# Kernel tuning notes

Hardware: AMD Instinct MI355X
Metric: run time of the kernel (lower is better)

## Reference

```python
import math
import jax, jax.numpy as jnp
import numpy as np
from jax import lax

B, IMG, CIN, ED, TD, M = 32, 224, 3, 64, 64, 32
DILATIONS = (1, 2, 3, 4)
KS, STRIDE = 7, 4


def _conv2d(x, w, b, stride, pad, dil=1):
    y = lax.conv_general_dilated(x, w, (stride, stride), [(pad, pad), (pad, pad)],
                                 rhs_dilation=(dil, dil),
                                 dimension_numbers=('NCHW', 'OIHW', 'NCHW'))
    return y + b[None, :, None, None]


def _ln(x, g, b):
    mu = x.mean(-1, keepdims=True)
    var = ((x - mu) ** 2).mean(-1, keepdims=True)
    return (x - mu) / jnp.sqrt(var + 1e-5) * g + b


def setup_inputs() -> dict:
    key = jax.random.key(0)
    ks = jax.random.split(key, 25)
    s = 0.05
    rn = lambda k, shp: (jax.random.normal(k, shp) * s).astype(jnp.float32)
    inp = {}
    inp['x'] = jax.random.normal(ks[0], (B, CIN, IMG, IMG), dtype=jnp.float32)
    # PRM dilated conv weights (stacked over 4 dilations)
    inp['prm_w'] = rn(ks[1], (4, ED, CIN, KS, KS))
    inp['prm_b'] = rn(ks[2], (4, ED))
    # PCM stem: conv-SiLU, conv-BN-SiLU, conv-SiLU
    inp['pcm_w1'] = rn(ks[3], (ED, CIN, 3, 3))
    inp['pcm_b1'] = rn(ks[4], (ED,))
    inp['pcm_w2'] = rn(ks[5], (ED, ED, 3, 3))
    inp['pcm_b2'] = rn(ks[6], (ED,))
    inp['bn_g'] = 1.0 + rn(ks[7], (ED,))
    inp['bn_b'] = rn(ks[8], (ED,))
    inp['bn_mean'] = rn(ks[9], (ED,))
    inp['bn_var'] = jax.random.uniform(ks[10], (ED,), minval=0.5, maxval=1.5).astype(jnp.float32)
    inp['pcm_w3'] = rn(ks[11], (TD, ED, 3, 3))
    inp['pcm_b3'] = rn(ks[12], (TD,))
    # Token_performer params (dim = 4*ED = 256, emb = TD = 64, m = 32)
    dim = 4 * ED
    inp['ln1_g'] = 1.0 + rn(ks[13], (dim,))
    inp['ln1_b'] = rn(ks[14], (dim,))
    inp['kqv_w'] = rn(ks[15], (3 * TD, dim))
    inp['kqv_b'] = rn(ks[16], (3 * TD,))
    # orthogonal random-feature matrix, rows orthonormal, scaled by sqrt(m)
    a = np.random.default_rng(0).normal(size=(TD, TD))
    qmat, _ = np.linalg.qr(a)
    inp['w_perf'] = jnp.asarray(qmat[:M] * math.sqrt(M), dtype=jnp.float32)
    inp['proj_w'] = rn(ks[17], (TD, TD))
    inp['proj_b'] = rn(ks[18], (TD,))
    inp['ln2_g'] = 1.0 + rn(ks[19], (TD,))
    inp['ln2_b'] = rn(ks[20], (TD,))
    inp['mlp_w1'] = rn(ks[21], (TD, TD))
    inp['mlp_b1'] = rn(ks[22], (TD,))
    inp['mlp_w2'] = rn(ks[23], (TD, TD))
    inp['mlp_b2'] = rn(ks[24], (TD,))
    inp['H'] = IMG
    inp['W'] = IMG
    return inp


def reference(x, prm_w, prm_b, pcm_w1, pcm_b1, pcm_w2, pcm_b2, bn_g, bn_b, bn_mean,
              bn_var, pcm_w3, pcm_b3, ln1_g, ln1_b, kqv_w, kqv_b, w_perf, proj_w,
              proj_b, ln2_g, ln2_b, mlp_w1, mlp_b1, mlp_w2, mlp_b2, H, W):
    Bx = x.shape[0]
    Hp, Wp = H // STRIDE, W // STRIDE
    # --- PRM: parallel dilated Conv2d + GELU branches ---
    branches = []
    for i, d in enumerate(DILATIONS):  # fixed small set of structurally distinct convs
        pad = math.ceil(((KS - 1) * d + 1 - STRIDE) / 2)
        branches.append(jax.nn.gelu(_conv2d(x, prm_w[i], prm_b[i], STRIDE, pad, d),
                                    approximate=False))
    y = jnp.stack(branches, axis=1)  # [B, 4, ED, Hp, Wp]
    prm_x = y.reshape(Bx, len(DILATIONS) * ED, Hp * Wp).transpose(0, 2, 1)  # [B, N, 256]
    # --- PCM stem: conv-SiLU / conv-BN-SiLU / conv-SiLU (eval-mode BN) ---
    c = jax.nn.silu(_conv2d(x, pcm_w1, pcm_b1, 2, 1))
    c = _conv2d(c, pcm_w2, pcm_b2, 2, 1)
    inv = (bn_g / jnp.sqrt(bn_var + 1e-5))[None, :, None, None]
    c = (c - bn_mean[None, :, None, None]) * inv + bn_b[None, :, None, None]
    c = jax.nn.silu(c)
    c = jax.nn.silu(_conv2d(c, pcm_w3, pcm_b3, 1, 1))  # [B, TD, Hp, Wp]
    convX = c.transpose(0, 2, 3, 1).reshape(Bx, Hp * Wp, TD)
    # --- Performer kernelized attention ---
    xn = _ln(prm_x, ln1_g, ln1_b)
    kqv = xn @ kqv_w.T + kqv_b
    k, q, v = kqv[..., :TD], kqv[..., TD:2 * TD], kqv[..., 2 * TD:]

    def prm_exp(z):
        xd = 0.5 * (z * z).sum(-1, keepdims=True)          # [B, N, 1]
        wtx = jnp.einsum('bti,mi->btm', z, w_perf)          # [B, N, M]
        return jnp.exp(wtx - xd) / math.sqrt(M)

    kp, qp = prm_exp(k), prm_exp(q)                         # [B, N, M]
    D = jnp.einsum('btm,bm->bt', qp, kp.sum(axis=1))[..., None]  # [B, N, 1]
    kptv = jnp.einsum('btn,btm->bnm', v, kp)                # [B, TD, M]
    ya = jnp.einsum('btm,bnm->btn', qp, kptv) / (D + 1e-8)  # [B, N, TD]
    ya = v + ya @ proj_w.T + proj_b
    # --- combine + MLP block ---
    xo = ya + convX
    h = _ln(xo, ln2_g, ln2_b)
    h = jax.nn.gelu(h @ mlp_w1.T + mlp_b1, approximate=False) @ mlp_w2.T + mlp_b2
    return xo + h
```

## Files before the change

### kernel.cpp

```cpp
#include <hip/hip_runtime.h>
#include <hip/hip_bf16.h>
#include <cstddef>

#define BB    32
#define IMG   224
#define CIN   3
#define ED    64
#define TD    64
#define MM    32
#define HP    56
#define TT    3136
#define C4    256
#define KQVN  192

typedef __attribute__((ext_vector_type(8))) short bf16x8;
typedef __attribute__((ext_vector_type(4))) float f32x4;

#define OFF_CONVX  0u
#define OFF_XN     6422528u
#define OFF_C2B    6422528u
#define OFF_C1B    19267584u
#define OFF_V      19267584u
#define OFF_KP     25690112u
#define OFF_QP     28901376u
#define OFF_PART   32112640u
#define OFF_KPTV   33161216u
#define OFF_KPSP   (OFF_KPTV + 32768u)
#define OFF_WPJB   (OFF_KPTV + 49152u)
#define OFF_WM1B   (OFF_KPTV + 51200u)
#define OFF_WM2B   (OFF_KPTV + 53248u)
#define OFF_WPFH   (OFF_KPTV + 55296u)
#define OFF_WPFL   (OFF_KPTV + 56320u)
#define OFF_KPSUM  33226752u
#define OFF_WPT    (OFF_PART)
#define OFF_WKB    (OFF_PART + 37632u)
#define OFF_WC2B   (OFF_PART + 62208u)
#define OFF_WT3B   (OFF_PART + 80640u)
#define OFF_WC1B   (OFF_PART + 99072u)

__device__ __forceinline__ float geluf(float v){
  return 0.5f*v*(1.f + erff(v*0.70710678118654752f));
}
__device__ __forceinline__ float siluf(float v){
// ... 42 lines not shown
  } else if (idx < 162560){
    int i5 = idx - 160512;
    int oc = i5 >> 5, k = i5 & 31;
    float v = 0.f;
    if (k < 27) v = pcm_w1[oc*27 + k];
    wc1b[i5] = __float2bfloat16(v);
  } else if (idx < 166656){
    wpjb[idx - 162560] = __float2bfloat16(proj_w[idx - 162560]);
  } else if (idx < 170752){
    wm1b[idx - 166656] = __float2bfloat16(mlp_w1[idx - 166656]);
  } else if (idx < 174848){
    wm2b[idx - 170752] = __float2bfloat16(mlp_w2[idx - 170752]);
  } else if (idx < 176896){
    int i6 = idx - 174848;
    wpfh[i6] = __float2bfloat16(wperf[i6]);
  } else if (idx < 178944){
    int i7 = idx - 176896;
    float v = wperf[i7];
    float h = bf2f(bfbits(v));
    wpfl[i7] = __float2bfloat16(v - h);
  }
}

__global__ __launch_bounds__(256) void k_conv1(
    const float* __restrict__ x, const __hip_bfloat16* __restrict__ wc1b,
    const float* __restrict__ bias, __hip_bfloat16* __restrict__ c1b)
{
  __shared__ __align__(16) ushort xs[3*17*18];
  __shared__ __align__(16) ushort As[64*40];
  const int t = threadIdx.x;
  const int b = blockIdx.y;
  const int th = blockIdx.x/14, tw = blockIdx.x - th*14;
  const int oh0 = th*8, ow0 = tw*8;
  const int ih0 = oh0*2 - 1, iw0 = ow0*2 - 1;
  const int w = t>>6, lane = t&63, l15 = lane&15, hi = lane>>4;

  const float* xb = x + (size_t)b*CIN*IMG*IMG;
  for (int idx = t; idx < 918; idx += 256){
    int ci = idx/306, rem = idx - ci*306;
    int r = rem/18, c = rem - r*18;
    float v = 0.f;
    int ih = ih0 + r, iw = iw0 + c;
    if (c < 17 && (unsigned)ih < 224u && (unsigned)iw < 224u)
      v = xb[(ci*IMG+ih)*IMG+iw];
    xs[idx] = bfbits(v);
  }
  __syncthreads();
  for (int idx = t; idx < 2048; idx += 256){
    int pos = idx >> 5, k = idx & 31;
    ushort v = 0;
    if (k < 27){
      int ci = k/9, rem = k - ci*9;
      int kh = rem/3, kw = rem - kh*3;
      v = xs[(ci*17 + (pos>>3)*2 + kh)*18 + (pos&7)*2 + kw];
    }
    As[pos*40 + k] = v;
  }
  __syncthreads();

  float bs4[4];
  #pragma unroll
  for (int nb=0;nb<4;++nb) bs4[nb] = bias[nb*16+l15];
  f32x4 acc[4];
  #pragma unroll
  for (int nb=0;nb<4;++nb) acc[nb] = (f32x4){0.f,0.f,0.f,0.f};
  const ushort* wq = (const ushort*)wc1b;
  {
    bf16x8 a = *(const bf16x8*)&As[(w*16+l15)*40 + hi*8];
    #pragma unroll
    for (int nb=0;nb<4;++nb){
      bf16x8 bv = *(const bf16x8*)&wq[(nb*16+l15)*32 + hi*8];
      acc[nb] = __builtin_amdgcn_mfma_f32_16x16x32_bf16(a, bv, acc[nb], 0, 0, 0);
    }
  }
  #pragma unroll
  for (int nb=0;nb<4;++nb){
    #pragma unroll
    for (int r=0;r<4;++r){
      int row = w*16 + hi*4 + r;
      int oh = oh0 + (row>>3), ow = ow0 + (row&7);
      c1b[(((size_t)b*112+oh)*112+ow)*64 + nb*16+l15] =
        __float2bfloat16(siluf(acc[nb][r] + bs4[nb]));
    }
  }
}

__global__ __launch_bounds__(256) void k_conv2(
    const __hip_bfloat16* __restrict__ c1b, const __hip_bfloat16* __restrict__ wc2b,
    const float* __restrict__ bias, const float* __restrict__ g,
    const float* __restrict__ bb, const float* __restrict__ mean,
    const float* __restrict__ var, __hip_bfloat16* __restrict__ c2b)
{
  __shared__ __align__(16) ushort xs[17*17*72];
  const int b = blockIdx.y;
  const int th = blockIdx.x/7, tw = blockIdx.x - th*7;
  const int oh0 = th*8, ow0 = tw*8;
  const int t = threadIdx.x;
  const int w = t>>6, lane = t&63, l15 = lane&15, hi = lane>>4;

  const int ih0 = oh0*2-1, iw0 = ow0*2-1;
  const ushort* c1u = (const ushort*)c1b;
  for (int seg = t; seg < 2312; seg += 256){
    int pos = seg >> 3, s8 = seg & 7;
    int r = pos/17, c = pos - r*17;
    int ih = ih0 + r, iw = iw0 + c;
    uint4 val = {0,0,0,0};
    if ((unsigned)ih < 112u && (unsigned)iw < 112u)
      val = *(const uint4*)&c1u[(((size_t)b*112+ih)*112+iw)*64 + s8*8];
    *(uint4*)&xs[(r*17+c)*72 + s8*8] = val;
  }
  __syncthreads();

  float bs4[4], iv4[4], mn4[4], bo4[4];
  #pragma unroll
  for (int nb=0;nb<4;++nb){
    int oc = nb*16+l15;
    bs4[nb] = bias[oc];
    iv4[nb] = g[oc]*rsqrtf(var[oc]+1e-5f);
    mn4[nb] = mean[oc];
    bo4[nb] = bb[oc];
  }

  f32x4 acc[4];
  #pragma unroll
  for (int nb=0;nb<4;++nb) acc[nb] = (f32x4){0.f,0.f,0.f,0.f};

  const int p = w*16 + l15, pr = p>>3, pc = p&7;
  const ushort* wq = (const ushort*)wc2b;

  for (int ks=0; ks<18; ++ks){
    const int k0 = ks*32 + hi*8;
    const int khkw = k0 >> 6, ci0 = k0 & 63;
    const int kh = khkw/3, kw = khkw - kh*3;
    bf16x8 a = *(const bf16x8*)&xs[((2*pr+kh)*17 + 2*pc+kw)*72 + ci0];
    #pragma unroll
    for (int nb=0;nb<4;++nb){
      bf16x8 bv = *(const bf16x8*)&wq[(nb*16+l15)*576 + k0];
      acc[nb] = __builtin_amdgcn_mfma_f32_16x16x32_bf16(a, bv, acc[nb], 0, 0, 0);
    }
  }

  #pragma unroll
  for (int nb=0;nb<4;++nb){
    #pragma unroll
    for (int r=0;r<4;++r){
      int pp = w*16 + hi*4 + r;
      int oh = oh0 + (pp>>3), ow = ow0 + (pp&7);
      float vv = acc[nb][r] + bs4[nb];
      vv = (vv - mn4[nb])*iv4[nb] + bo4[nb];
      c2b[(((size_t)b*56+oh)*56+ow)*64 + nb*16+l15] = __float2bfloat16(siluf(vv));
    }
  }
}

__global__ __launch_bounds__(256) void k_conv3(
    const __hip_bfloat16* __restrict__ c2b, const __hip_bfloat16* __restrict__ wt3b,
    const float* __restrict__ bias, __hip_bfloat16* __restrict__ convXb)
{
  __shared__ __align__(16) ushort xs[10*12*72];
  const int b = blockIdx.y;
  const int th = blockIdx.x/7, tw = blockIdx.x - th*7;
  const int oh0 = th*8, ow0 = tw*8;
  const int t = threadIdx.x;
  const int w = t>>6, lane = t&63, l15 = lane&15, hi = lane>>4;

  const ushort* c2u = (const ushort*)c2b;
  for (int seg = t; seg < 960; seg += 256){
    int pos = seg >> 3, s8 = seg & 7;
    int r = pos/12, c = pos - r*12;
    int ih = oh0 - 1 + r, iw = ow0 - 1 + c;
    uint4 val = {0,0,0,0};
    if ((unsigned)ih < 56u && (unsigned)iw < 56u)
      val = *(const uint4*)&c2u[(((size_t)b*56+ih)*56+iw)*64 + s8*8];
    *(uint4*)&xs[(r*12+c)*72 + s8*8] = val;
  }
  __syncthreads();

  float bs4[4];
  #pragma unroll
  for (int nb=0;nb<4;++nb) bs4[nb] = bias[nb*16+l15];

  f32x4 acc[4];
  #pragma unroll
  for (int nb=0;nb<4;++nb) acc[nb] = (f32x4){0.f,0.f,0.f,0.f};

  const int p = w*16 + l15, pr = p>>3, pc = p&7;
  const ushort* wq = (const ushort*)wt3b;

  for (int ks=0; ks<18; ++ks){
    const int k0 = ks*32 + hi*8;
    const int khkw = k0 >> 6, ci0 = k0 & 63;
    const int kh = khkw/3, kw = khkw - kh*3;
    bf16x8 a = *(const bf16x8*)&xs[((pr+kh)*12 + pc+kw)*72 + ci0];
    #pragma unroll
    for (int nb=0;nb<4;++nb){
      bf16x8 bv = *(const bf16x8*)&wq[(nb*16+l15)*576 + k0];
      acc[nb] = __builtin_amdgcn_mfma_f32_16x16x32_bf16(a, bv, acc[nb], 0, 0, 0);
    }
  }

  #pragma unroll
  for (int nb=0;nb<4;++nb){
    #pragma unroll
    for (int r=0;r<4;++r){
      int pp = w*16 + hi*4 + r;
      int oh = oh0 + (pp>>3), ow = ow0 + (pp&7);
      int s = oh*HP + ow;
      convXb[((size_t)b*TT + s)*64 + nb*16+l15] =
        __float2bfloat16(siluf(acc[nb][r] + bs4[nb]));
    }
  }
}

#define LOADX(PH) do{ const float4* xr_ = (const float4*)(rowb + (PH)*20); \
  *(float4*)&X[0]=xr_[0]; *(float4*)&X[4]=xr_[1]; *(float4*)&X[8]=xr_[2]; \
  *(float4*)&X[12]=xr_[3]; *(float4*)&X[16]=xr_[4]; }while(0)
#define TAP(KW,Q0) do{ const float wv_ = wrow[(KW)*64]; \
  v[0]+=wv_*X[(Q0)+0];  v[1]+=wv_*X[(Q0)+1];  v[2]+=wv_*X[(Q0)+2];  v[3]+=wv_*X[(Q0)+3]; \
  v[4]+=wv_*X[(Q0)+4];  v[5]+=wv_*X[(Q0)+5];  v[6]+=wv_*X[(Q0)+6];  v[7]+=wv_*X[(Q0)+7]; \
  v[8]+=wv_*X[(Q0)+8];  v[9]+=wv_*X[(Q0)+9];  v[10]+=wv_*X[(Q0)+10]; v[11]+=wv_*X[(Q0)+11]; \
  v[12]+=wv_*X[(Q0)+12]; v[13]+=wv_*X[(Q0)+13]; }while(0)

template<int D>
__device__ __forceinline__ void prm_core(const float* __restrict__ xt2,
    const float* __restrict__ wq, float v[14])
{
  constexpr int R0 = 12 - 3*D;
  #pragma unroll 1
  for (int ci=0; ci<3; ++ci){
    #pragma unroll 1
    for (int kh=0; kh<7; ++kh){
      const float* rowb = xt2 + ci*2000 + (R0 + kh*D)*80;
      const float* wrow = wq + ((ci*7+kh)*7)*64;
      float X[20];
      if constexpr (D == 1){
        LOADX(0); TAP(3,3);
        LOADX(1); TAP(0,2); TAP(4,3);
        LOADX(2); TAP(1,2); TAP(5,3);
        LOADX(3); TAP(2,2); TAP(6,3);
      } else if constexpr (D == 2){
        LOADX(0); TAP(1,2); TAP(3,3); TAP(5,4);
        LOADX(2); TAP(0,1); TAP(2,2); TAP(4,3); TAP(6,4);
      } else if constexpr (D == 3){
        LOADX(0); TAP(3,3);
        LOADX(1); TAP(2,2); TAP(6,5);
        LOADX(2); TAP(1,1); TAP(5,4);
        LOADX(3); TAP(0,0); TAP(4,3);
      } else {
        LOADX(0); TAP(0,0); TAP(1,1); TAP(2,2); TAP(3,3); TAP(4,4); TAP(5,5); TAP(6,6);
      }
    }
  }
}

__global__ __launch_bounds__(256) void k_prm_ln(
    const float* __restrict__ x, const float* __restrict__ wpt,
    const float* __restrict__ prm_b, const float* __restrict__ ln_g,
    const float* __restrict__ ln_b, __hip_bfloat16* __restrict__ xn, int b0)
{
  __shared__ __align__(16) float xt2[6000];
  __shared__ float wred[4][14][2];
  const int t = threadIdx.x;
  const int b = blockIdx.y + b0;
  const int oh  = blockIdx.x >> 2;
  const int owt = blockIdx.x & 3;
  const int ow0 = owt*14;
  const int ih0 = oh*4 - 11;
  const int iw0 = ow0*4 - 11;

  const float* xb = x + (size_t)b*CIN*IMG*IMG;
  for (int idx = t; idx < 6000; idx += 256){
    int ci  = idx / 2000;
    int rem = idx - ci*2000;
    int r   = rem / 80;
    int cc  = rem - r*80;
    int ih = ih0 + r, iw = iw0 + cc;
    float val = 0.f;
    if ((unsigned)ih < (unsigned)IMG && (unsigned)iw < (unsigned)IMG)
      val = xb[(ci*IMG+ih)*IMG+iw];
    xt2[(ci*25 + r)*80 + (cc&3)*20 + (cc>>2)] = val;
  }
  __syncthreads();

  const int i = t >> 6, lane = t & 63;
  float v[14];
  const float bi = prm_b[i*64+lane];
  #pragma unroll
  for (int p=0;p<14;++p) v[p] = bi;
  const float* wq = wpt + (i*147)*64 + lane;

  if      (i == 0) prm_core<1>(xt2, wq, v);
  else if (i == 1) prm_core<2>(xt2, wq, v);
  else if (i == 2) prm_core<3>(xt2, wq, v);
  else             prm_core<4>(xt2, wq, v);

  #pragma unroll
  for (int p=0;p<14;++p) v[p] = geluf(v[p]);
  #pragma unroll
  for (int p=0;p<14;++p){
    float s1 = v[p], s2 = v[p]*v[p];
    #pragma unroll
    for (int o=32;o;o>>=1){
      s1 += __shfl_xor(s1, o, 64);
      s2 += __shfl_xor(s2, o, 64);
    }
    if (lane == 0){ wred[i][p][0] = s1; wred[i][p][1] = s2; }
  }
  __syncthreads();
  const float lg = ln_g[t], lb = ln_b[t];
  const int s_base = oh*HP + ow0;
  #pragma unroll
  for (int p=0;p<14;++p){
    float S1 = wred[0][p][0]+wred[1][p][0]+wred[2][p][0]+wred[3][p][0];
    float S2 = wred[0][p][1]+wred[1][p][1]+wred[2][p][1]+wred[3][p][1];
    float mu = S1*(1.f/256.f);
    float rs = rsqrtf(S2*(1.f/256.f) - mu*mu + 1e-5f);
    float outv = (v[p]-mu)*rs*lg + lb;
    xn[((size_t)(b*TT + s_base + p))*256 + t] = __float2bfloat16(outv);
  }
}

__global__ __launch_bounds__(256) void k_kqv_perf(
    const __hip_bfloat16* __restrict__ xn, const __hip_bfloat16* __restrict__ wkb,
    const float* __restrict__ kqv_b,
    const __hip_bfloat16* __restrict__ wpfh, const __hip_bfloat16* __restrict__ wpfl,
    float* __restrict__ v_g, float* __restrict__ kp, float* __restrict__ qp)
{
  __shared__ __align__(16) char smem[36864];
  __shared__ __align__(16) ushort wph[32*72];
  __shared__ __align__(16) ushort wpl[32*72];
  __shared__ float kqvb_s[192];
  __shared__ float xd_s[128];
  ushort* As  = (ushort*)smem;
  ushort* Bs  = (ushort*)(smem + 9216);
  ushort* zhb = (ushort*)smem;
  ushort* zlb = (ushort*)(smem + 18432);

  const int t = threadIdx.x;
  const int m0 = blockIdx.x*64;
  const int w = t >> 6, lane = t & 63;
  const int l15 = lane & 15, hi = lane >> 4;

  const ushort* wph_g = (const ushort*)wpfh;
  const ushort* wpl_g = (const ushort*)wpfl;
  for (int idx = t; idx < 2048; idx += 256){
    int row = idx >> 6, c = idx & 63;
    wph[row*72 + c] = wph_g[idx];
    wpl[row*72 + c] = wpl_g[idx];
  }
// ... 29 lines not shown
      for (int nb=0;nb<12;++nb){
        bf16x8 bv = *(const bf16x8*)&Bs[(nb*16 + l15)*72 + ks*32 + hi*8];
        acc[nb] = __builtin_amdgcn_mfma_f32_16x16x32_bf16(a, bv, acc[nb], 0, 0, 0);
      }
    }
    __syncthreads();
  }

  #pragma unroll
  for (int nb=0;nb<12;++nb){
    int col = nb*16 + l15;
    float bias = kqvb_s[col];
    #pragma unroll
    for (int r=0;r<4;++r){
      int row = w*16 + hi*4 + r;
      float val = acc[nb][r] + bias;
      if (col < 128){
        int zrow = (col >> 6)*64 + row;
        int zc = col & 63;
        ushort zh = bfbits(val);
        zhb[zrow*72 + zc] = zh;
        zlb[zrow*72 + zc] = bfbits(val - bf2f(zh));
      } else {
        v_g[((size_t)(m0+row))*64 + (col-128)] = val;
      }
    }
  }
  __syncthreads();

  if (t < 128){
    float s = 0.f;
    #pragma unroll
    for (int c8=0;c8<8;++c8){
      bf16x8 zh8 = *(const bf16x8*)&zhb[t*72 + c8*8];
      bf16x8 zl8 = *(const bf16x8*)&zlb[t*72 + c8*8];
      #pragma unroll
      for (int j=0;j<8;++j){
        float z = bf2f((ushort)zh8[j]) + bf2f((ushort)zl8[j]);
        s += z*z;
      }
    }
    xd_s[t] = 0.5f*s;
  }
  __syncthreads();

  f32x4 accd[2][2];
  #pragma unroll
// ... 8 lines not shown
      bf16x8 ah = *(const bf16x8*)&zhb[(rb*16 + l15)*72 + ks*32 + hi*8];
      bf16x8 al = *(const bf16x8*)&zlb[(rb*16 + l15)*72 + ks*32 + hi*8];
      #pragma unroll
      for (int nb=0;nb<2;++nb){
        bf16x8 bh = *(const bf16x8*)&wph[(nb*16 + l15)*72 + ks*32 + hi*8];
        bf16x8 bl = *(const bf16x8*)&wpl[(nb*16 + l15)*72 + ks*32 + hi*8];
        accd[ri][nb] = __builtin_amdgcn_mfma_f32_16x16x32_bf16(ah, bh, accd[ri][nb], 0, 0, 0);
        accd[ri][nb] = __builtin_amdgcn_mfma_f32_16x16x32_bf16(al, bh, accd[ri][nb], 0, 0, 0);
        accd[ri][nb] = __builtin_amdgcn_mfma_f32_16x16x32_bf16(ah, bl, accd[ri][nb], 0, 0, 0);
      }
    }
  }
  #pragma unroll
  for (int ri=0;ri<2;++ri){
    const int rb = 2*w + ri;
    #pragma unroll
    for (int nb=0;nb<2;++nb){
      const int m = nb*16 + l15;
      #pragma unroll
      for (int r=0;r<4;++r){
        int row = rb*16 + hi*4 + r;
        int wh = row >> 6, pos = row & 63;
        float outv = expf(accd[ri][nb][r] - xd_s[row]) * 0.17677669529663687f;
        float* dst = wh ? qp : kp;
        dst[((size_t)(m0+pos))*32 + m] = outv;
      }
    }
  }
}

__global__ __launch_bounds__(256) void k_kptv(
    const float* __restrict__ v_g, const float* __restrict__ kp,
    float* __restrict__ part, float* __restrict__ kpsum_part)
{
  __shared__ __align__(16) ushort vT[64*232];
  __shared__ __align__(16) ushort kpT[32*232];
  __shared__ float ksh[8][32];
  const int b = blockIdx.y, g = blockIdx.x;
  const int t = threadIdx.x;
  const int w = t>>6, lane = t&63, l15 = lane&15, hi = lane>>4;
  const int t0 = g*196;

  for (int idx = t; idx < 14336; idx += 256){
    int tt = idx >> 6, n = idx & 63;
    float vv = (tt < 196) ? v_g[((size_t)b*TT + t0 + tt)*64 + n] : 0.f;
    vT[n*232 + tt] = bfbits(vv);
  }
  for (int idx = t; idx < 7168; idx += 256){
    int tt = idx >> 5, m = idx & 31;
    float kv = (tt < 196) ? kp[((size_t)b*TT + t0 + tt)*32 + m] : 0.f;
    kpT[m*232 + tt] = bfbits(kv);
  }
  __syncthreads();

  f32x4 accp[2];
  accp[0] = (f32x4){0.f,0.f,0.f,0.f};
  accp[1] = (f32x4){0.f,0.f,0.f,0.f};
  for (int ks=0; ks<7; ++ks){
    bf16x8 a = *(const bf16x8*)&vT[(w*16+l15)*232 + ks*32 + hi*8];
    #pragma unroll
    for (int nt=0; nt<2; ++nt){
      bf16x8 bv = *(const bf16x8*)&kpT[(nt*16+l15)*232 + ks*32 + hi*8];
      accp[nt] = __builtin_amdgcn_mfma_f32_16x16x32_bf16(a, bv, accp[nt], 0, 0, 0);
    }
  }
  #pragma unroll
  for (int nt=0;nt<2;++nt){
    #pragma unroll
    for (int r=0;r<4;++r){
      int row = w*16 + hi*4 + r;
      int col = nt*16 + l15;
      part[(((size_t)g*BB + b)*64 + row)*MM + col] = accp[nt][r];
    }
  }
  {
    int m = t & 31, h8 = t >> 5;
    float s = 0.f;
    int lo = h8*25, hic = lo+25 < 196 ? lo+25 : 196;
    for (int tt = lo; tt < hic; ++tt){
      s += bf2f(kpT[m*232 + tt]);
    }
    ksh[h8][m] = s;
  }
  __syncthreads();
  if (t < 32){
    float s = 0.f;
    #pragma unroll
    for (int j=0;j<8;++j) s += ksh[j][t];
    kpsum_part[(size_t)g*1024 + b*32 + t] = s;
  }
}

__global__ __launch_bounds__(256) void k_kptv_red(
    const float* __restrict__ part, const float* __restrict__ kpsum_part,
    __hip_bfloat16* __restrict__ kptvb, float* __restrict__ kpsum)
{
  const int t = threadIdx.x;
  const int idx = blockIdx.x*256 + t;
  float a = 0.f;
  #pragma unroll
  for (int g=0; g<16; ++g) a += part[(size_t)g*65536 + idx];
  kptvb[idx] = __float2bfloat16(a);
  if (blockIdx.x < 4){
    int kidx = blockIdx.x*256 + t;
    float s = 0.f;
    #pragma unroll
    for (int g=0; g<16; ++g) s += kpsum_part[(size_t)g*1024 + kidx];
    kpsum[kidx] = s;
  }
}

__global__ __launch_bounds__(256) void k_attn_mlp(
    const float* __restrict__ v_g, const float* __restrict__ qp,
    const float* __restrict__ kpsum, const __hip_bfloat16* __restrict__ kptvb,
    const __hip_bfloat16* __restrict__ wpjb, const float* __restrict__ projb,
    const __hip_bfloat16* __restrict__ convXb,
    const float* __restrict__ ln2_g, const float* __restrict__ ln2_b,
    const __hip_bfloat16* __restrict__ wm1b, const float* __restrict__ b1,
    const __hip_bfloat16* __restrict__ wm2b, const float* __restrict__ b2,
    float* __restrict__ out)
{
  __shared__ __align__(16) char smem[64512];
  ushort* qpb = (ushort*)smem;
  ushort* ktb = (ushort*)(smem + 5120);
  ushort* pjw = (ushort*)(smem + 10240);
  ushort* hb  = (ushort*)smem;
  ushort* t2  = (ushort*)(smem + 19456);
  ushort* w1b = (ushort*)(smem + 28672);
  ushort* w2b = (ushort*)(smem + 37888);
  float*  xosh= (float*)(smem + 47104);
  __shared__ float Ds[64];
  __shared__ float Dp[4][64];
  __shared__ float ks_s[32], pjb_s[64], b1_s[64], b2_s[64], g2_s[64], bb2_s[64];

  const int t = threadIdx.x;
  const int b = blockIdx.y;
  const int p0 = blockIdx.x*64;
  const int w = t>>6, lane = t&63, l15 = lane&15, hi = lane>>4;

  const float* qpg = qp + ((size_t)b*TT + p0)*32;
  for (int idx = t; idx < 2048; idx += 256)
    qpb[(idx>>5)*40 + (idx&31)] = bfbits(qpg[idx]);
  const ushort* ktg = (const ushort*)kptvb + (size_t)b*2048;
  for (int idx = t; idx < 2048; idx += 256)
    ktb[(idx>>5)*40 + (idx&31)] = ktg[idx];
  const ushort* pju = (const ushort*)wpjb;
  const ushort* w1u = (const ushort*)wm1b;
  const ushort* w2u = (const ushort*)wm2b;
  for (int idx = t; idx < 4096; idx += 256){
    pjw[(idx>>6)*72 + (idx&63)] = pju[idx];
    w1b[(idx>>6)*72 + (idx&63)] = w1u[idx];
    w2b[(idx>>6)*72 + (idx&63)] = w2u[idx];
  }
  if (t < 32) ks_s[t] = kpsum[b*MM + t];
  if (t < 64){
    pjb_s[t] = projb[t]; b1_s[t] = b1[t]; b2_s[t] = b2[t];
    g2_s[t] = ln2_g[t];  bb2_s[t] = ln2_b[t];
  }
  __syncthreads();

  {
    int pos = t & 63, grp = t >> 6;
    float s = 0.f;
    #pragma unroll
    for (int j=0;j<8;++j){
// ... 20 lines not shown
  #pragma unroll
  for (int nb=0;nb<4;++nb){
    #pragma unroll
    for (int r=0;r<4;++r){
      int row = w*16 + hi*4 + r;
      t2[row*72 + nb*16 + l15] = bfbits(acc1[nb][r] / Ds[row]);
    }
  }
  __syncthreads();

  f32x4 acc2[4];
  #pragma unroll
  for (int nb=0;nb<4;++nb) acc2[nb] = (f32x4){0.f,0.f,0.f,0.f};
  #pragma unroll
  for (int ks=0; ks<2; ++ks){
    bf16x8 a2 = *(const bf16x8*)&t2[(w*16 + l15)*72 + ks*32 + hi*8];
    #pragma unroll
    for (int nb=0;nb<4;++nb){
      bf16x8 bv2 = *(const bf16x8*)&pjw[(nb*16 + l15)*72 + ks*32 + hi*8];
      acc2[nb] = __builtin_amdgcn_mfma_f32_16x16x32_bf16(a2, bv2, acc2[nb], 0, 0, 0);
    }
  }
  const ushort* cxu = (const ushort*)convXb;
  #pragma unroll
  for (int nb=0;nb<4;++nb){
    #pragma unroll
    for (int r=0;r<4;++r){
      int row = w*16 + hi*4 + r;
      int col = nb*16 + l15;
      const size_t off = ((size_t)b*TT + p0 + row)*64 + col;
      xosh[row*68 + col] = v_g[off] + acc2[nb][r] + pjb_s[col] + bf2f(cxu[off]);
    }
  }
  __syncthreads();

  {
    const int n = t & 63, p = t >> 6;
    const float g2 = g2_s[n], bb2 = bb2_s[n];
    for (int sp=0; sp<16; ++sp){
      const int pos = sp*4 + p;
      const float xv = xosh[pos*68 + n];
      float s1 = xv, s2 = xv*xv;
      #pragma unroll
      for (int o=32;o;o>>=1){
        s1 += __shfl_xor(s1, o, 64);
        s2 += __shfl_xor(s2, o, 64);
      }
      float mu = s1*(1.f/64.f);
      float rs = rsqrtf(s2*(1.f/64.f) - mu*mu + 1e-5f);
      t2[pos*72 + n] = bfbits((xv - mu)*rs*g2 + bb2);
    }
  }
  __syncthreads();

// ... 58 lines not shown
  const float* pcm_b2 = (const float*)d_in[6];
  const float* bn_g   = (const float*)d_in[7];
  const float* bn_b   = (const float*)d_in[8];
  const float* bn_mean= (const float*)d_in[9];
  const float* bn_var = (const float*)d_in[10];
  const float* pcm_w3 = (const float*)d_in[11];
  const float* pcm_b3 = (const float*)d_in[12];
  const float* ln1_g  = (const float*)d_in[13];
  const float* ln1_b  = (const float*)d_in[14];
  const float* kqv_w  = (const float*)d_in[15];
  const float* kqv_b  = (const float*)d_in[16];
  const float* w_perf = (const float*)d_in[17];
  const float* proj_w = (const float*)d_in[18];
  const float* proj_b = (const float*)d_in[19];
  const float* ln2_g  = (const float*)d_in[20];
  const float* ln2_b  = (const float*)d_in[21];
  const float* mlp_w1 = (const float*)d_in[22];
  const float* mlp_b1 = (const float*)d_in[23];
  const float* mlp_w2 = (const float*)d_in[24];
  const float* mlp_b2 = (const float*)d_in[25];

  float* ws = (float*)d_ws;
  __hip_bfloat16* convXb = (__hip_bfloat16*)(ws + OFF_CONVX);
  __hip_bfloat16* xn  = (__hip_bfloat16*)(ws + OFF_XN);
  __hip_bfloat16* c2b = (__hip_bfloat16*)(ws + OFF_C2B);
  __hip_bfloat16* c1b = (__hip_bfloat16*)(ws + OFF_C1B);
  float* v_g   = ws + OFF_V;
  float* kp    = ws + OFF_KP;
  float* qp    = ws + OFF_QP;
  float* part  = ws + OFF_PART;
  __hip_bfloat16* kptvb = (__hip_bfloat16*)(ws + OFF_KPTV);
  float* kpsum_part = ws + OFF_KPSP;
  float* kpsum = ws + OFF_KPSUM;
  float* wpt   = ws + OFF_WPT;
  __hip_bfloat16* wkb  = (__hip_bfloat16*)(ws + OFF_WKB);
  __hip_bfloat16* wc2b = (__hip_bfloat16*)(ws + OFF_WC2B);
  __hip_bfloat16* wt3b = (__hip_bfloat16*)(ws + OFF_WT3B);
  __hip_bfloat16* wc1b = (__hip_bfloat16*)(ws + OFF_WC1B);
  __hip_bfloat16* wpjb = (__hip_bfloat16*)(ws + OFF_WPJB);
  __hip_bfloat16* wm1b = (__hip_bfloat16*)(ws + OFF_WM1B);
  __hip_bfloat16* wm2b = (__hip_bfloat16*)(ws + OFF_WM2B);
  __hip_bfloat16* wpfh = (__hip_bfloat16*)(ws + OFF_WPFH);
  __hip_bfloat16* wpfl = (__hip_bfloat16*)(ws + OFF_WPFL);
  float* out   = (float*)d_out;

  k_wtrans<<<dim3(699), 256, 0, stream>>>(prm_w, kqv_w, pcm_w2, pcm_w3, pcm_w1,
                                          proj_w, mlp_w1, mlp_w2, w_perf,
                                          wpt, wkb, wc2b, wt3b, wc1b,
                                          wpjb, wm1b, wm2b, wpfh, wpfl);
  k_conv1<<<dim3(196,BB), 256, 0, stream>>>(x, wc1b, pcm_b1, c1b);
  k_conv2<<<dim3(49,BB), 256, 0, stream>>>(c1b, wc2b, pcm_b2, bn_g, bn_b,
                                           bn_mean, bn_var, c2b);
  k_conv3<<<dim3(49,BB), 256, 0, stream>>>(c2b, wt3b, pcm_b3, convXb);
  k_prm_ln<<<dim3(224,16), 256, 0, stream>>>(x, wpt, prm_b, ln1_g, ln1_b, xn, 0);
  k_prm_ln<<<dim3(224,16), 256, 0, stream>>>(x, wpt, prm_b, ln1_g, ln1_b, xn, 16);
  k_kqv_perf<<<dim3(1568), 256, 0, stream>>>(xn, wkb, kqv_b, wpfh, wpfl, v_g, kp, qp);
  k_kptv<<<dim3(16,BB), 256, 0, stream>>>(v_g, kp, part, kpsum_part);
  k_kptv_red<<<dim3(256), 256, 0, stream>>>(part, kpsum_part, kptvb, kpsum);
  k_attn_mlp<<<dim3(49,BB), 256, 0, stream>>>(v_g, qp, kpsum, kptvb, wpjb, proj_b,
                                              convXb, ln2_g, ln2_b, wm1b, mlp_b1,
                                              wm2b, mlp_b2, out);
}
```

Baseline: 484.9 us.

## Merge PRM and conv1 into one launch; store v, kp, qp as bf16

Result: slower. 497.8 us (+2.7%).

```diff
diff --git a/kernel.cpp b/kernel.cpp
--- a/kernel.cpp
+++ b/kernel.cpp
@@ -17,8 +17,8 @@
 typedef __attribute__((ext_vector_type(4))) float f32x4;
 
 #define OFF_CONVX  0u
+#define OFF_C2B    3211264u
 #define OFF_XN     6422528u
-#define OFF_C2B    6422528u
 #define OFF_C1B    19267584u
 #define OFF_V      19267584u
 #define OFF_KP     25690112u
@@ -107,196 +107,6 @@
   }
 }
 
-__global__ __launch_bounds__(256) void k_conv1(
-    const float* __restrict__ x, const __hip_bfloat16* __restrict__ wc1b,
-    const float* __restrict__ bias, __hip_bfloat16* __restrict__ c1b)
-{
-  __shared__ __align__(16) ushort xs[3*17*18];
-  __shared__ __align__(16) ushort As[64*40];
-  const int t = threadIdx.x;
-  const int b = blockIdx.y;
-  const int th = blockIdx.x/14, tw = blockIdx.x - th*14;
-  const int oh0 = th*8, ow0 = tw*8;
-  const int ih0 = oh0*2 - 1, iw0 = ow0*2 - 1;
-  const int w = t>>6, lane = t&63, l15 = lane&15, hi = lane>>4;
-
-  const float* xb = x + (size_t)b*CIN*IMG*IMG;
-  for (int idx = t; idx < 918; idx += 256){
-    int ci = idx/306, rem = idx - ci*306;
-    int r = rem/18, c = rem - r*18;
-    float v = 0.f;
-    int ih = ih0 + r, iw = iw0 + c;
-    if (c < 17 && (unsigned)ih < 224u && (unsigned)iw < 224u)
-      v = xb[(ci*IMG+ih)*IMG+iw];
-    xs[idx] = bfbits(v);
-  }
-  __syncthreads();
-  for (int idx = t; idx < 2048; idx += 256){
-    int pos = idx >> 5, k = idx & 31;
-    ushort v = 0;
-    if (k < 27){
-      int ci = k/9, rem = k - ci*9;
-      int kh = rem/3, kw = rem - kh*3;
-      v = xs[(ci*17 + (pos>>3)*2 + kh)*18 + (pos&7)*2 + kw];
-    }
-    As[pos*40 + k] = v;
-  }
-  __syncthreads();
-
-  float bs4[4];
-  #pragma unroll
-  for (int nb=0;nb<4;++nb) bs4[nb] = bias[nb*16+l15];
-  f32x4 acc[4];
-  #pragma unroll
-  for (int nb=0;nb<4;++nb) acc[nb] = (f32x4){0.f,0.f,0.f,0.f};
-  const ushort* wq = (const ushort*)wc1b;
-  {
-    bf16x8 a = *(const bf16x8*)&As[(w*16+l15)*40 + hi*8];
-    #pragma unroll
-    for (int nb=0;nb<4;++nb){
-      bf16x8 bv = *(const bf16x8*)&wq[(nb*16+l15)*32 + hi*8];
-      acc[nb] = __builtin_amdgcn_mfma_f32_16x16x32_bf16(a, bv, acc[nb], 0, 0, 0);
-    }
-  }
-  #pragma unroll
-  for (int nb=0;nb<4;++nb){
-    #pragma unroll
-    for (int r=0;r<4;++r){
-      int row = w*16 + hi*4 + r;
-      int oh = oh0 + (row>>3), ow = ow0 + (row&7);
-      c1b[(((size_t)b*112+oh)*112+ow)*64 + nb*16+l15] =
-        __float2bfloat16(siluf(acc[nb][r] + bs4[nb]));
-    }
-  }
-}
-
-__global__ __launch_bounds__(256) void k_conv2(
-    const __hip_bfloat16* __restrict__ c1b, const __hip_bfloat16* __restrict__ wc2b,
-    const float* __restrict__ bias, const float* __restrict__ g,
-    const float* __restrict__ bb, const float* __restrict__ mean,
-    const float* __restrict__ var, __hip_bfloat16* __restrict__ c2b)
-{
-  __shared__ __align__(16) ushort xs[17*17*72];
-  const int b = blockIdx.y;
-  const int th = blockIdx.x/7, tw = blockIdx.x - th*7;
-  const int oh0 = th*8, ow0 = tw*8;
-  const int t = threadIdx.x;
-  const int w = t>>6, lane = t&63, l15 = lane&15, hi = lane>>4;
-
-  const int ih0 = oh0*2-1, iw0 = ow0*2-1;
-  const ushort* c1u = (const ushort*)c1b;
-  for (int seg = t; seg < 2312; seg += 256){
-    int pos = seg >> 3, s8 = seg & 7;
-    int r = pos/17, c = pos - r*17;
-    int ih = ih0 + r, iw = iw0 + c;
-    uint4 val = {0,0,0,0};
-    if ((unsigned)ih < 112u && (unsigned)iw < 112u)
-      val = *(const uint4*)&c1u[(((size_t)b*112+ih)*112+iw)*64 + s8*8];
-    *(uint4*)&xs[(r*17+c)*72 + s8*8] = val;
-  }
-  __syncthreads();
-
-  float bs4[4], iv4[4], mn4[4], bo4[4];
-  #pragma unroll
-  for (int nb=0;nb<4;++nb){
-    int oc = nb*16+l15;
-    bs4[nb] = bias[oc];
-    iv4[nb] = g[oc]*rsqrtf(var[oc]+1e-5f);
-    mn4[nb] = mean[oc];
-    bo4[nb] = bb[oc];
-  }
-
-  f32x4 acc[4];
-  #pragma unroll
-  for (int nb=0;nb<4;++nb) acc[nb] = (f32x4){0.f,0.f,0.f,0.f};
-
-  const int p = w*16 + l15, pr = p>>3, pc = p&7;
-  const ushort* wq = (const ushort*)wc2b;
-
-  for (int ks=0; ks<18; ++ks){
-    const int k0 = ks*32 + hi*8;
-    const int khkw = k0 >> 6, ci0 = k0 & 63;
-    const int kh = khkw/3, kw = khkw - kh*3;
-    bf16x8 a = *(const bf16x8*)&xs[((2*pr+kh)*17 + 2*pc+kw)*72 + ci0];
-    #pragma unroll
-    for (int nb=0;nb<4;++nb){
-      bf16x8 bv = *(const bf16x8*)&wq[(nb*16+l15)*576 + k0];
-      acc[nb] = __builtin_amdgcn_mfma_f32_16x16x32_bf16(a, bv, acc[nb], 0, 0, 0);
-    }
-  }
-
-  #pragma unroll
-  for (int nb=0;nb<4;++nb){
-    #pragma unroll
-    for (int r=0;r<4;++r){
-      int pp = w*16 + hi*4 + r;
-      int oh = oh0 + (pp>>3), ow = ow0 + (pp&7);
-      float vv = acc[nb][r] + bs4[nb];
-      vv = (vv - mn4[nb])*iv4[nb] + bo4[nb];
-      c2b[(((size_t)b*56+oh)*56+ow)*64 + nb*16+l15] = __float2bfloat16(siluf(vv));
-    }
-  }
-}
-
-__global__ __launch_bounds__(256) void k_conv3(
-    const __hip_bfloat16* __restrict__ c2b, const __hip_bfloat16* __restrict__ wt3b,
-    const float* __restrict__ bias, __hip_bfloat16* __restrict__ convXb)
-{
-  __shared__ __align__(16) ushort xs[10*12*72];
-  const int b = blockIdx.y;
-  const int th = blockIdx.x/7, tw = blockIdx.x - th*7;
-  const int oh0 = th*8, ow0 = tw*8;
-  const int t = threadIdx.x;
-  const int w = t>>6, lane = t&63, l15 = lane&15, hi = lane>>4;
-
-  const ushort* c2u = (const ushort*)c2b;
-  for (int seg = t; seg < 960; seg += 256){
-    int pos = seg >> 3, s8 = seg & 7;
-    int r = pos/12, c = pos - r*12;
-    int ih = oh0 - 1 + r, iw = ow0 - 1 + c;
-    uint4 val = {0,0,0,0};
-    if ((unsigned)ih < 56u && (unsigned)iw < 56u)
-      val = *(const uint4*)&c2u[(((size_t)b*56+ih)*56+iw)*64 + s8*8];
-    *(uint4*)&xs[(r*12+c)*72 + s8*8] = val;
-  }
-  __syncthreads();
-
-  float bs4[4];
-  #pragma unroll
-  for (int nb=0;nb<4;++nb) bs4[nb] = bias[nb*16+l15];
-
-  f32x4 acc[4];
-  #pragma unroll
-  for (int nb=0;nb<4;++nb) acc[nb] = (f32x4){0.f,0.f,0.f,0.f};
-
-  const int p = w*16 + l15, pr = p>>3, pc = p&7;
-  const ushort* wq = (const ushort*)wt3b;
-
-  for (int ks=0; ks<18; ++ks){
-    const int k0 = ks*32 + hi*8;
-    const int khkw = k0 >> 6, ci0 = k0 & 63;
-    const int kh = khkw/3, kw = khkw - kh*3;
-    bf16x8 a = *(const bf16x8*)&xs[((pr+kh)*12 + pc+kw)*72 + ci0];
-    #pragma unroll
-    for (int nb=0;nb<4;++nb){
-      bf16x8 bv = *(const bf16x8*)&wq[(nb*16+l15)*576 + k0];
-      acc[nb] = __builtin_amdgcn_mfma_f32_16x16x32_bf16(a, bv, acc[nb], 0, 0, 0);
-    }
-  }
-
-  #pragma unroll
-  for (int nb=0;nb<4;++nb){
-    #pragma unroll
-    for (int r=0;r<4;++r){
-      int pp = w*16 + hi*4 + r;
-      int oh = oh0 + (pp>>3), ow = ow0 + (pp&7);
-      int s = oh*HP + ow;
-      convXb[((size_t)b*TT + s)*64 + nb*16+l15] =
-        __float2bfloat16(siluf(acc[nb][r] + bs4[nb]));
-    }
-  }
-}
-
 #define LOADX(PH) do{ const float4* xr_ = (const float4*)(rowb + (PH)*20); \
   *(float4*)&X[0]=xr_[0]; *(float4*)&X[4]=xr_[1]; *(float4*)&X[8]=xr_[2]; \
   *(float4*)&X[12]=xr_[3]; *(float4*)&X[16]=xr_[4]; }while(0)
@@ -338,70 +148,263 @@
   }
 }
 
-__global__ __launch_bounds__(256) void k_prm_ln(
+__global__ __launch_bounds__(256) void k_prm_conv1(
     const float* __restrict__ x, const float* __restrict__ wpt,
     const float* __restrict__ prm_b, const float* __restrict__ ln_g,
-    const float* __restrict__ ln_b, __hip_bfloat16* __restrict__ xn, int b0)
-{
-  __shared__ __align__(16) float xt2[6000];
+    const float* __restrict__ ln_b, __hip_bfloat16* __restrict__ xn,
+    const __hip_bfloat16* __restrict__ wc1b, const float* __restrict__ c1bias,
+    __hip_bfloat16* __restrict__ c1b)
+{
+  __shared__ __align__(16) char fsm[24448];
   __shared__ float wred[4][14][2];
   const int t = threadIdx.x;
-  const int b = blockIdx.y + b0;
-  const int oh  = blockIdx.x >> 2;
-  const int owt = blockIdx.x & 3;
-  const int ow0 = owt*14;
-  const int ih0 = oh*4 - 11;
-  const int iw0 = ow0*4 - 11;
-
-  const float* xb = x + (size_t)b*CIN*IMG*IMG;
-  for (int idx = t; idx < 6000; idx += 256){
-    int ci  = idx / 2000;
-    int rem = idx - ci*2000;
-    int r   = rem / 80;
-    int cc  = rem - r*80;
-    int ih = ih0 + r, iw = iw0 + cc;
-    float val = 0.f;
-    if ((unsigned)ih < (unsigned)IMG && (unsigned)iw < (unsigned)IMG)
-      val = xb[(ci*IMG+ih)*IMG+iw];
-    xt2[(ci*25 + r)*80 + (cc&3)*20 + (cc>>2)] = val;
-  }
-  __syncthreads();
-
-  const int i = t >> 6, lane = t & 63;
-  float v[14];
-  const float bi = prm_b[i*64+lane];
-  #pragma unroll
-  for (int p=0;p<14;++p) v[p] = bi;
-  const float* wq = wpt + (i*147)*64 + lane;
-
-  if      (i == 0) prm_core<1>(xt2, wq, v);
-  else if (i == 1) prm_core<2>(xt2, wq, v);
-  else if (i == 2) prm_core<3>(xt2, wq, v);
-  else             prm_core<4>(xt2, wq, v);
-
-  #pragma unroll
-  for (int p=0;p<14;++p) v[p] = geluf(v[p]);
-  #pragma unroll
-  for (int p=0;p<14;++p){
-    float s1 = v[p], s2 = v[p]*v[p];
-    #pragma unroll
-    for (int o=32;o;o>>=1){
-      s1 += __shfl_xor(s1, o, 64);
-      s2 += __shfl_xor(s2, o, 64);
-    }
-    if (lane == 0){ wred[i][p][0] = s1; wred[i][p][1] = s2; }
-  }
-  __syncthreads();
-  const float lg = ln_g[t], lb = ln_b[t];
-  const int s_base = oh*HP + ow0;
-  #pragma unroll
-  for (int p=0;p<14;++p){
-    float S1 = wred[0][p][0]+wred[1][p][0]+wred[2][p][0]+wred[3][p][0];
-    float S2 = wred[0][p][1]+wred[1][p][1]+wred[2][p][1]+wred[3][p][1];
-    float mu = S1*(1.f/256.f);
-    float rs = rsqrtf(S2*(1.f/256.f) - mu*mu + 1e-5f);
-    float outv = (v[p]-mu)*rs*lg + lb;
-    xn[((size_t)(b*TT + s_base + p))*256 + t] = __float2bfloat16(outv);
+  const int group = blockIdx.x/15, r15 = blockIdx.x - group*15;
+
+  if (r15 < 8){
+    float* xt2 = (float*)fsm;
+    const int pid = group*8 + r15;
+    const int b = pid/224, rest = pid - b*224;
+    const int oh  = rest >> 2;
+    const int owt = rest & 3;
+    const int ow0 = owt*14;
+    const int ih0 = oh*4 - 11;
+    const int iw0 = ow0*4 - 11;
+
+    const float* xb = x + (size_t)b*CIN*IMG*IMG;
+    for (int idx = t; idx < 6000; idx += 256){
+      int ci  = idx / 2000;
+      int rem = idx - ci*2000;
+      int r   = rem / 80;
+      int cc  = rem - r*80;
+      int ih = ih0 + r, iw = iw0 + cc;
+      float val = 0.f;
+      if ((unsigned)ih < (unsigned)IMG && (unsigned)iw < (unsigned)IMG)
+        val = xb[(ci*IMG+ih)*IMG+iw];
+      xt2[(ci*25 + r)*80 + (cc&3)*20 + (cc>>2)] = val;
+    }
+    __syncthreads();
+
+    const int i = t >> 6, lane = t & 63;
+    float v[14];
+    const float bi = prm_b[i*64+lane];
+    #pragma unroll
+    for (int p=0;p<14;++p) v[p] = bi;
+    const float* wq = wpt + (i*147)*64 + lane;
+
+    if      (i == 0) prm_core<1>(xt2, wq, v);
+    else if (i == 1) prm_core<2>(xt2, wq, v);
+    else if (i == 2) prm_core<3>(xt2, wq, v);
+    else             prm_core<4>(xt2, wq, v);
+
+    #pragma unroll
+    for (int p=0;p<14;++p) v[p] = geluf(v[p]);
+    #pragma unroll
+    for (int p=0;p<14;++p){
+      float s1 = v[p], s2 = v[p]*v[p];
+      #pragma unroll
+      for (int o=32;o;o>>=1){
+        s1 += __shfl_xor(s1, o, 64);
+        s2 += __shfl_xor(s2, o, 64);
+      }
+      if (lane == 0){ wred[i][p][0] = s1; wred[i][p][1] = s2; }
+    }
+    __syncthreads();
+    const float lg = ln_g[t], lb = ln_b[t];
+    const int s_base = oh*HP + ow0;
+    #pragma unroll
+    for (int p=0;p<14;++p){
+      float S1 = wred[0][p][0]+wred[1][p][0]+wred[2][p][0]+wred[3][p][0];
+      float S2 = wred[0][p][1]+wred[1][p][1]+wred[2][p][1]+wred[3][p][1];
+      float mu = S1*(1.f/256.f);
+      float rs = rsqrtf(S2*(1.f/256.f) - mu*mu + 1e-5f);
+      float outv = (v[p]-mu)*rs*lg + lb;
+      xn[((size_t)(b*TT + s_base + p))*256 + t] = __float2bfloat16(outv);
+    }
+  } else {
+    ushort* xs = (ushort*)fsm;
+    ushort* As = (ushort*)(fsm + 4096);
+    const int cid = group*7 + (r15 - 8);
+    const int b = cid/196, s196 = cid - b*196;
+    const int th = s196/14, tw = s196 - th*14;
+    const int oh0 = th*8, ow0 = tw*8;
+    const int ih0 = oh0*2 - 1, iw0 = ow0*2 - 1;
+    const int w = t>>6, lane = t&63, l15 = lane&15, hi = lane>>4;
+
+    const float* xb = x + (size_t)b*CIN*IMG*IMG;
+    for (int idx = t; idx < 918; idx += 256){
+      int ci = idx/306, rem = idx - ci*306;
+      int r = rem/18, c = rem - r*18;
+      float v = 0.f;
+      int ih = ih0 + r, iw = iw0 + c;
+      if (c < 17 && (unsigned)ih < 224u && (unsigned)iw < 224u)
+        v = xb[(ci*IMG+ih)*IMG+iw];
+      xs[idx] = bfbits(v);
+    }
+    __syncthreads();
+    for (int idx = t; idx < 2048; idx += 256){
+      int pos = idx >> 5, k = idx & 31;
+      ushort v = 0;
+      if (k < 27){
+        int ci = k/9, rem = k - ci*9;
+        int kh = rem/3, kw = rem - kh*3;
+        v = xs[(ci*17 + (pos>>3)*2 + kh)*18 + (pos&7)*2 + kw];
+      }
+      As[pos*40 + k] = v;
+    }
+    __syncthreads();
+
+    float bs4[4];
+    #pragma unroll
+    for (int nb=0;nb<4;++nb) bs4[nb] = c1bias[nb*16+l15];
+    f32x4 acc[4];
+    #pragma unroll
+    for (int nb=0;nb<4;++nb) acc[nb] = (f32x4){0.f,0.f,0.f,0.f};
+    const ushort* wq = (const ushort*)wc1b;
+    {
+      bf16x8 a = *(const bf16x8*)&As[(w*16+l15)*40 + hi*8];
+      #pragma unroll
+      for (int nb=0;nb<4;++nb){
+        bf16x8 bv = *(const bf16x8*)&wq[(nb*16+l15)*32 + hi*8];
+        acc[nb] = __builtin_amdgcn_mfma_f32_16x16x32_bf16(a, bv, acc[nb], 0, 0, 0);
+      }
+    }
+    #pragma unroll
+    for (int nb=0;nb<4;++nb){
+      #pragma unroll
+      for (int r=0;r<4;++r){
+        int row = w*16 + hi*4 + r;
+        int oh = oh0 + (row>>3), ow = ow0 + (row&7);
+        c1b[(((size_t)b*112+oh)*112+ow)*64 + nb*16+l15] =
+          __float2bfloat16(siluf(acc[nb][r] + bs4[nb]));
+      }
+    }
+  }
+}
+
+__global__ __launch_bounds__(256) void k_conv2(
+    const __hip_bfloat16* __restrict__ c1b, const __hip_bfloat16* __restrict__ wc2b,
+    const float* __restrict__ bias, const float* __restrict__ g,
+    const float* __restrict__ bb, const float* __restrict__ mean,
+    const float* __restrict__ var, __hip_bfloat16* __restrict__ c2b)
+{
+  __shared__ __align__(16) ushort xs[17*17*72];
+  const int b = blockIdx.y;
+  const int th = blockIdx.x/7, tw = blockIdx.x - th*7;
+  const int oh0 = th*8, ow0 = tw*8;
+  const int t = threadIdx.x;
+  const int w = t>>6, lane = t&63, l15 = lane&15, hi = lane>>4;
+
+  const int ih0 = oh0*2-1, iw0 = ow0*2-1;
+  const ushort* c1u = (const ushort*)c1b;
+  for (int seg = t; seg < 2312; seg += 256){
+    int pos = seg >> 3, s8 = seg & 7;
+    int r = pos/17, c = pos - r*17;
+    int ih = ih0 + r, iw = iw0 + c;
+    uint4 val = {0,0,0,0};
+    if ((unsigned)ih < 112u && (unsigned)iw < 112u)
+      val = *(const uint4*)&c1u[(((size_t)b*112+ih)*112+iw)*64 + s8*8];
+    *(uint4*)&xs[(r*17+c)*72 + s8*8] = val;
+  }
+  __syncthreads();
+
+  float bs4[4], iv4[4], mn4[4], bo4[4];
+  #pragma unroll
+  for (int nb=0;nb<4;++nb){
+    int oc = nb*16+l15;
+    bs4[nb] = bias[oc];
+    iv4[nb] = g[oc]*rsqrtf(var[oc]+1e-5f);
+    mn4[nb] = mean[oc];
+    bo4[nb] = bb[oc];
+  }
+
+  f32x4 acc[4];
+  #pragma unroll
+  for (int nb=0;nb<4;++nb) acc[nb] = (f32x4){0.f,0.f,0.f,0.f};
+
+  const int p = w*16 + l15, pr = p>>3, pc = p&7;
+  const ushort* wq = (const ushort*)wc2b;
+
+  for (int ks=0; ks<18; ++ks){
+    const int k0 = ks*32 + hi*8;
+    const int khkw = k0 >> 6, ci0 = k0 & 63;
+    const int kh = khkw/3, kw = khkw - kh*3;
+    bf16x8 a = *(const bf16x8*)&xs[((2*pr+kh)*17 + 2*pc+kw)*72 + ci0];
+    #pragma unroll
+    for (int nb=0;nb<4;++nb){
+      bf16x8 bv = *(const bf16x8*)&wq[(nb*16+l15)*576 + k0];
+      acc[nb] = __builtin_amdgcn_mfma_f32_16x16x32_bf16(a, bv, acc[nb], 0, 0, 0);
+    }
+  }
+
+  #pragma unroll
+  for (int nb=0;nb<4;++nb){
+    #pragma unroll
+    for (int r=0;r<4;++r){
+      int pp = w*16 + hi*4 + r;
+      int oh = oh0 + (pp>>3), ow = ow0 + (pp&7);
+      float vv = acc[nb][r] + bs4[nb];
+      vv = (vv - mn4[nb])*iv4[nb] + bo4[nb];
+      c2b[(((size_t)b*56+oh)*56+ow)*64 + nb*16+l15] = __float2bfloat16(siluf(vv));
+    }
+  }
+}
+
+__global__ __launch_bounds__(256) void k_conv3(
+    const __hip_bfloat16* __restrict__ c2b, const __hip_bfloat16* __restrict__ wt3b,
+    const float* __restrict__ bias, __hip_bfloat16* __restrict__ convXb)
+{
+  __shared__ __align__(16) ushort xs[10*12*72];
+  const int b = blockIdx.y;
+  const int th = blockIdx.x/7, tw = blockIdx.x - th*7;
+  const int oh0 = th*8, ow0 = tw*8;
+  const int t = threadIdx.x;
+  const int w = t>>6, lane = t&63, l15 = lane&15, hi = lane>>4;
+
+  const ushort* c2u = (const ushort*)c2b;
+  for (int seg = t; seg < 960; seg += 256){
+    int pos = seg >> 3, s8 = seg & 7;
+    int r = pos/12, c = pos - r*12;
+    int ih = oh0 - 1 + r, iw = ow0 - 1 + c;
+    uint4 val = {0,0,0,0};
+    if ((unsigned)ih < 56u && (unsigned)iw < 56u)
+      val = *(const uint4*)&c2u[(((size_t)b*56+ih)*56+iw)*64 + s8*8];
+    *(uint4*)&xs[(r*12+c)*72 + s8*8] = val;
+  }
+  __syncthreads();
+
+  float bs4[4];
+  #pragma unroll
+  for (int nb=0;nb<4;++nb) bs4[nb] = bias[nb*16+l15];
+
+  f32x4 acc[4];
+  #pragma unroll
+  for (int nb=0;nb<4;++nb) acc[nb] = (f32x4){0.f,0.f,0.f,0.f};
+
+  const int p = w*16 + l15, pr = p>>3, pc = p&7;
+  const ushort* wq = (const ushort*)wt3b;
+
+  for (int ks=0; ks<18; ++ks){
+    const int k0 = ks*32 + hi*8;
+    const int khkw = k0 >> 6, ci0 = k0 & 63;
+    const int kh = khkw/3, kw = khkw - kh*3;
+    bf16x8 a = *(const bf16x8*)&xs[((pr+kh)*12 + pc+kw)*72 + ci0];
+    #pragma unroll
+    for (int nb=0;nb<4;++nb){
+      bf16x8 bv = *(const bf16x8*)&wq[(nb*16+l15)*576 + k0];
+      acc[nb] = __builtin_amdgcn_mfma_f32_16x16x32_bf16(a, bv, acc[nb], 0, 0, 0);
+    }
+  }
+
+  #pragma unroll
+  for (int nb=0;nb<4;++nb){
+    #pragma unroll
+    for (int r=0;r<4;++r){
+      int pp = w*16 + hi*4 + r;
+      int oh = oh0 + (pp>>3), ow = ow0 + (pp&7);
+      int s = oh*HP + ow;
+      convXb[((size_t)b*TT + s)*64 + nb*16+l15] =
+        __float2bfloat16(siluf(acc[nb][r] + bs4[nb]));
+    }
   }
 }
 
@@ -409,7 +412,8 @@
     const __hip_bfloat16* __restrict__ xn, const __hip_bfloat16* __restrict__ wkb,
     const float* __restrict__ kqv_b,
     const __hip_bfloat16* __restrict__ wpfh, const __hip_bfloat16* __restrict__ wpfl,
-    float* __restrict__ v_g, float* __restrict__ kp, float* __restrict__ qp)
+    __hip_bfloat16* __restrict__ v_g, __hip_bfloat16* __restrict__ kp,
+    __hip_bfloat16* __restrict__ qp)
 {
   __shared__ __align__(16) char smem[36864];
   __shared__ __align__(16) ushort wph[32*72];
@@ -485,7 +489,7 @@
         zhb[zrow*72 + zc] = zh;
         zlb[zrow*72 + zc] = bfbits(val - bf2f(zh));
       } else {
-        v_g[((size_t)(m0+row))*64 + (col-128)] = val;
+        ((ushort*)v_g)[((size_t)(m0+row))*64 + (col-128)] = bfbits(val);
       }
     }
   }
@@ -540,15 +544,15 @@
         int row = rb*16 + hi*4 + r;
         int wh = row >> 6, pos = row & 63;
         float outv = expf(accd[ri][nb][r] - xd_s[row]) * 0.17677669529663687f;
-        float* dst = wh ? qp : kp;
-        dst[((size_t)(m0+pos))*32 + m] = outv;
+        ushort* dst = (ushort*)(wh ? qp : kp);
+        dst[((size_t)(m0+pos))*32 + m] = bfbits(outv);
       }
     }
   }
 }
 
 __global__ __launch_bounds__(256) void k_kptv(
-    const float* __restrict__ v_g, const float* __restrict__ kp,
+    const __hip_bfloat16* __restrict__ v_g, const __hip_bfloat16* __restrict__ kp,
     float* __restrict__ part, float* __restrict__ kpsum_part)
 {
   __shared__ __align__(16) ushort vT[64*232];
@@ -558,16 +562,16 @@
   const int t = threadIdx.x;
   const int w = t>>6, lane = t&63, l15 = lane&15, hi = lane>>4;
   const int t0 = g*196;
+  const ushort* vu = (const ushort*)v_g;
+  const ushort* ku = (const ushort*)kp;
 
   for (int idx = t; idx < 14336; idx += 256){
     int tt = idx >> 6, n = idx & 63;
-    float vv = (tt < 196) ? v_g[((size_t)b*TT + t0 + tt)*64 + n] : 0.f;
-    vT[n*232 + tt] = bfbits(vv);
+    vT[n*232 + tt] = (tt < 196) ? vu[((size_t)b*TT + t0 + tt)*64 + n] : (ushort)0;
   }
   for (int idx = t; idx < 7168; idx += 256){
     int tt = idx >> 5, m = idx & 31;
-    float kv = (tt < 196) ? kp[((size_t)b*TT + t0 + tt)*32 + m] : 0.f;
-    kpT[m*232 + tt] = bfbits(kv);
+    kpT[m*232 + tt] = (tt < 196) ? ku[((size_t)b*TT + t0 + tt)*32 + m] : (ushort)0;
   }
   __syncthreads();
 
@@ -595,9 +599,7 @@
     int m = t & 31, h8 = t >> 5;
     float s = 0.f;
     int lo = h8*25, hic = lo+25 < 196 ? lo+25 : 196;
-    for (int tt = lo; tt < hic; ++tt){
-      s += bf2f(kpT[m*232 + tt]);
-    }
+    for (int tt = lo; tt < hic; ++tt) s += bf2f(kpT[m*232 + tt]);
     ksh[h8][m] = s;
   }
   __syncthreads();
@@ -629,7 +631,7 @@
 }
 
 __global__ __launch_bounds__(256) void k_attn_mlp(
-    const float* __restrict__ v_g, const float* __restrict__ qp,
+    const __hip_bfloat16* __restrict__ v_g, const __hip_bfloat16* __restrict__ qp,
     const float* __restrict__ kpsum, const __hip_bfloat16* __restrict__ kptvb,
     const __hip_bfloat16* __restrict__ wpjb, const float* __restrict__ projb,
     const __hip_bfloat16* __restrict__ convXb,
@@ -656,9 +658,9 @@
   const int p0 = blockIdx.x*64;
   const int w = t>>6, lane = t&63, l15 = lane&15, hi = lane>>4;
 
-  const float* qpg = qp + ((size_t)b*TT + p0)*32;
+  const ushort* qpu = (const ushort*)qp + ((size_t)b*TT + p0)*32;
   for (int idx = t; idx < 2048; idx += 256)
-    qpb[(idx>>5)*40 + (idx&31)] = bfbits(qpg[idx]);
+    qpb[(idx>>5)*40 + (idx&31)] = qpu[idx];
   const ushort* ktg = (const ushort*)kptvb + (size_t)b*2048;
   for (int idx = t; idx < 2048; idx += 256)
     ktb[(idx>>5)*40 + (idx&31)] = ktg[idx];
@@ -725,6 +727,7 @@
     }
   }
   const ushort* cxu = (const ushort*)convXb;
+  const ushort* vu  = (const ushort*)v_g;
   #pragma unroll
   for (int nb=0;nb<4;++nb){
     #pragma unroll
@@ -732,7 +735,7 @@
       int row = w*16 + hi*4 + r;
       int col = nb*16 + l15;
       const size_t off = ((size_t)b*TT + p0 + row)*64 + col;
-      xosh[row*68 + col] = v_g[off] + acc2[nb][r] + pjb_s[col] + bf2f(cxu[off]);
+      xosh[row*68 + col] = bf2f(vu[off]) + acc2[nb][r] + pjb_s[col] + bf2f(cxu[off]);
     }
   }
   __syncthreads();
@@ -837,12 +840,12 @@
 
   float* ws = (float*)d_ws;
   __hip_bfloat16* convXb = (__hip_bfloat16*)(ws + OFF_CONVX);
+  __hip_bfloat16* c2b = (__hip_bfloat16*)(ws + OFF_C2B);
   __hip_bfloat16* xn  = (__hip_bfloat16*)(ws + OFF_XN);
-  __hip_bfloat16* c2b = (__hip_bfloat16*)(ws + OFF_C2B);
   __hip_bfloat16* c1b = (__hip_bfloat16*)(ws + OFF_C1B);
-  float* v_g   = ws + OFF_V;
-  float* kp    = ws + OFF_KP;
-  float* qp    = ws + OFF_QP;
+  __hip_bfloat16* v_g = (__hip_bfloat16*)(ws + OFF_V);
+  __hip_bfloat16* kp  = (__hip_bfloat16*)(ws + OFF_KP);
+  __hip_bfloat16* qp  = (__hip_bfloat16*)(ws + OFF_QP);
   float* part  = ws + OFF_PART;
   __hip_bfloat16* kptvb = (__hip_bfloat16*)(ws + OFF_KPTV);
   float* kpsum_part = ws + OFF_KPSP;
@@ -863,12 +866,11 @@
                                           proj_w, mlp_w1, mlp_w2, w_perf,
                                           wpt, wkb, wc2b, wt3b, wc1b,
                                           wpjb, wm1b, wm2b, wpfh, wpfl);
-  k_conv1<<<dim3(196,BB), 256, 0, stream>>>(x, wc1b, pcm_b1, c1b);
+  k_prm_conv1<<<dim3(13440), 256, 0, stream>>>(x, wpt, prm_b, ln1_g, ln1_b, xn,
+                                               wc1b, pcm_b1, c1b);
   k_conv2<<<dim3(49,BB), 256, 0, stream>>>(c1b, wc2b, pcm_b2, bn_g, bn_b,
                                            bn_mean, bn_var, c2b);
   k_conv3<<<dim3(49,BB), 256, 0, stream>>>(c2b, wt3b, pcm_b3, convXb);
-  k_prm_ln<<<dim3(224,16), 256, 0, stream>>>(x, wpt, prm_b, ln1_g, ln1_b, xn, 0);
-  k_prm_ln<<<dim3(224,16), 256, 0, stream>>>(x, wpt, prm_b, ln1_g, ln1_b, xn, 16);
   k_kqv_perf<<<dim3(1568), 256, 0, stream>>>(xn, wkb, kqv_b, wpfh, wpfl, v_g, kp, qp);
   k_kptv<<<dim3(16,BB), 256, 0, stream>>>(v_g, kp, part, kpsum_part);
   k_kptv_red<<<dim3(256), 256, 0, stream>>>(part, kpsum_part, kptvb, kpsum);
```
